# Kernel optimization log

Hardware: AMD Instinct MI355X
Metric: run time of the kernel (lower is better)

Reference implementation:

```python
import jax, jax.numpy as jnp
import numpy as np

N = 100000   # num nodes
E = 1000000  # num edges
IN = 64      # in_channels
H = 64       # hidden_dim
RESCUE_SCALE = 0.01


def setup_inputs() -> dict:
    key = jax.random.key(0)
    ks = jax.random.split(key, 8)
    x = jax.random.normal(ks[0], (N, IN), jnp.float32)
    edge_index = jax.random.randint(ks[1], (2, E), 0, N, dtype=jnp.int64)
    edge_weight = jax.random.uniform(ks[2], (E,), jnp.float32)
    glorot = lambda k, sh, fan: jax.random.normal(k, sh, jnp.float32) / np.sqrt(fan).astype(np.float32)
    W1 = glorot(ks[3], (IN, H), IN); b1 = jnp.zeros((H,), jnp.float32)
    W2 = glorot(ks[4], (H, H), H);  b2 = jnp.zeros((H,), jnp.float32)
    Wn = glorot(ks[5], (H, 1), H);  bn = jnp.zeros((1,), jnp.float32)
    Wr = glorot(ks[6], (H, 1), H);  br = jnp.zeros((1,), jnp.float32)
    return {"x": x, "edge_index": edge_index, "edge_weight": edge_weight,
            "W1": W1, "b1": b1, "W2": W2, "b2": b2,
            "Wn": Wn, "bn": bn, "Wr": Wr, "br": br}


def gcn_conv(x, src, dst, ew, W, b):
    # PyG GCNConv: linear first, then symmetric-normalized scatter-add aggregation.
    x = x @ W                                              # [N, H]
    deg = jax.ops.segment_sum(ew, dst, num_segments=N)     # weighted in-degree
    dinv = jnp.where(deg > 0, jax.lax.rsqrt(deg), 0.0)     # deg^{-1/2}, inf -> 0
    norm = dinv[src] * ew * dinv[dst]                      # [E+N]
    out = jax.ops.segment_sum(x[src] * norm[:, None], dst, num_segments=N)
    return out + b


def reference(x, edge_index, edge_weight, W1, b1, W2, b2, Wn, bn, Wr, br):
    # add self-loops with weight 1 (GCNConv default)
    loop = jnp.arange(N, dtype=edge_index.dtype)
    src = jnp.concatenate([edge_index[0], loop])
    dst = jnp.concatenate([edge_index[1], loop])
    ew = jnp.concatenate([edge_weight, jnp.ones((N,), edge_weight.dtype)])

    h = jax.nn.relu(gcn_conv(x, src, dst, ew, W1, b1))
    h = jax.nn.relu(gcn_conv(h, src, dst, ew, W2, b2))

    node_logits = (h @ Wn + bn).squeeze(-1)                # [N]
    node_selector = jax.nn.softmax(node_logits, axis=0)
    rescue_ratios = jax.nn.sigmoid((h @ Wr + br).squeeze(-1)) * RESCUE_SCALE
    return node_selector, rescue_ratios
```

## Files before the change

kernel.cpp:

```cpp
#include <hip/hip_runtime.h>
#include <hip/hip_fp16.h>
#include <math.h>

#define NN 100000
#define NE 1000000
#define CAP 32
#define OVCAP 4096
#define NEB 3907
#define NT32 3125
#define RB 256
#define GB1 512

typedef _Float16 half8 __attribute__((ext_vector_type(8)));
typedef float f32x4 __attribute__((ext_vector_type(4)));


__device__ __forceinline__ void stage_B_lds(const float* __restrict__ W,
                                            _Float16* __restrict__ ldsB) {
  for (int u = threadIdx.x; u < 512; u += 256) {
    int slane = u & 63, ts = u >> 6;
    int t = ts >> 1, s = ts & 1;
    int qq = slane >> 4, ll = slane & 15;
#pragma unroll
    for (int j = 0; j < 8; ++j)
      ldsB[u * 8 + j] = (_Float16)W[(s * 32 + qq * 8 + j) * 64 + t * 16 + ll];
  }
}


__global__ __launch_bounds__(256) void k_bucket_gemm1(const int* __restrict__ src,
                                                      const int* __restrict__ dst,
                                                      const float* __restrict__ ew,
                                                      const float* __restrict__ X,
                                                      const float* __restrict__ W1,
                                                      int* __restrict__ cnt,
                                                      int2* __restrict__ bucket,
                                                      int4* __restrict__ ovf,
                                                      int* __restrict__ ovf_n,
                                                      __half* __restrict__ Y) {
  __shared__ _Float16 ldsB[4096];
  if (blockIdx.x >= GB1) {
    int e = (blockIdx.x - GB1) * 256 + threadIdx.x;
    if (e < NE) {
      int s = src[e];
      int d = dst[e];
      float w = ew[e];
      int pos = atomicAdd(&cnt[d], 1);
      if (pos < CAP) {
        bucket[d * CAP + pos] = make_int2(s, __float_as_int(w));
      } else {
        int t = atomicAdd(ovf_n, 1);
        if (t < OVCAP) ovf[t] = make_int4(s, d, __float_as_int(w), 0);
      }
    }
    return;
  }
  stage_B_lds(W1, ldsB);
  __syncthreads();
  int lane = threadIdx.x & 63;
  int l15 = lane & 15, q = lane >> 4;
  half8 bfr[4][2];
#pragma unroll
  for (int t = 0; t < 4; ++t)
#pragma unroll
    for (int s = 0; s < 2; ++s)
      bfr[t][s] = *(half8*)&ldsB[((t * 2 + s) * 64 + lane) * 8];

  int wid = blockIdx.x * 4 + (threadIdx.x >> 6);
  for (int tile = wid; tile < NN / 16; tile += GB1 * 4) {
    int row = tile * 16 + l15;
    f32x4 acc[4] = {{0.f,0.f,0.f,0.f},{0.f,0.f,0.f,0.f},
                    {0.f,0.f,0.f,0.f},{0.f,0.f,0.f,0.f}};
#pragma unroll
    for (int s = 0; s < 2; ++s) {
      const float* ap = X + (size_t)row * 64 + s * 32 + q * 8;
      float4 a0 = *(const float4*)ap;
      float4 a1 = *(const float4*)(ap + 4);
      half8 af;
      af[0] = (_Float16)a0.x; af[1] = (_Float16)a0.y;
      af[2] = (_Float16)a0.z; af[3] = (_Float16)a0.w;
      af[4] = (_Float16)a1.x; af[5] = (_Float16)a1.y;
      af[6] = (_Float16)a1.z; af[7] = (_Float16)a1.w;
#pragma unroll
      for (int t = 0; t < 4; ++t)
        acc[t] = __builtin_amdgcn_mfma_f32_16x16x32_f16(af, bfr[t][s], acc[t], 0, 0, 0);
    }
#pragma unroll
    for (int r = 0; r < 4; ++r) {
      int rw = tile * 16 + q * 4 + r;
#pragma unroll
      for (int t = 0; t < 4; ++t)
        Y[(size_t)rw * 64 + t * 16 + l15] = __float2half(acc[t][r]);
    }
  }
}


__global__ __launch_bounds__(256) void k_dinv(const int* __restrict__ cnt,
                                              const int2* __restrict__ bucket,
                                              const int4* __restrict__ ovf,
                                              const int* __restrict__ ovf_n,
                                              float* __restrict__ dinv) {
  int t = threadIdx.x & 3;
  int node = blockIdx.x * 64 + (threadIdx.x >> 2);
  if (node >= NN) return;
  int c = cnt[node];
  int cc = c < CAP ? c : CAP;
  int nq = (cc + 1) >> 1;
  const int4* bk4 = (const int4*)(bucket + (size_t)node * CAP);
  float dsum = 0.f;
  for (int j = t; j < nq; j += 4) {
    int4 qv = bk4[j];
    int e0 = 2 * j, e1 = 2 * j + 1;
    if (e0 < cc) dsum += __int_as_float(qv.y);
    if (e1 < cc) dsum += __int_as_float(qv.w);
  }
  dsum += __shfl_xor(dsum, 1, 64);
  dsum += __shfl_xor(dsum, 2, 64);
  if (t == 0) {
    float tot = dsum + 1.0f;
    if (c > CAP) {
      int on = ovf_n[0]; if (on > OVCAP) on = OVCAP;
      for (int k = 0; k < on; ++k) {
        int4 o = ovf[k];
        if (o.y == node) tot += __int_as_float(o.z);
      }
    }
    dinv[node] = 1.0f / sqrtf(tot);
  }
}


__device__ __forceinline__ void h8load(const __half* p, float4& a, float4& b) {
  float4 raw = *(const float4*)p;
  __half2 h0 = *(__half2*)&raw.x;
  __half2 h1 = *(__half2*)&raw.y;
  __half2 h2 = *(__half2*)&raw.z;
  __half2 h3 = *(__half2*)&raw.w;
  float2 f0 = __half22float2(h0), f1 = __half22float2(h1);
  float2 f2 = __half22float2(h2), f3 = __half22float2(h3);
  a = make_float4(f0.x, f0.y, f1.x, f1.y);
  b = make_float4(f2.x, f2.y, f3.x, f3.y);
}

#define FMA8(xa, xb, v) do { \
  A.x = fmaf((xa).x, (v), A.x); A.y = fmaf((xa).y, (v), A.y); \
  A.z = fmaf((xa).z, (v), A.z); A.w = fmaf((xa).w, (v), A.w); \
  B.x = fmaf((xb).x, (v), B.x); B.y = fmaf((xb).y, (v), B.y); \
  B.z = fmaf((xb).z, (v), B.z); B.w = fmaf((xb).w, (v), B.w); } while (0)

template <bool FOLD>
__device__ __forceinline__ void gather_node8(const __half* __restrict__ xw,
                                             const int* __restrict__ cnt,
                                             const int2* __restrict__ bucket,
                                             const int4* __restrict__ ovf,
                                             const int* __restrict__ ovf_n,
                                             const float* __restrict__ dinv,
                                             int node, int l, float selfw,
                                             float4& A, float4& B) {
  int c = cnt[node];
  int cc = c < CAP ? c : CAP;
  const int4* bk4 = (const int4*)(bucket + (size_t)node * CAP);
  A = make_float4(0.f, 0.f, 0.f, 0.f);
  B = make_float4(0.f, 0.f, 0.f, 0.f);

  int j = 0;
  for (; j + 4 <= cc; j += 4) {
    int4 pa = bk4[j >> 1];
    int4 pb = bk4[(j >> 1) + 1];
    float4 xa0, xb0, xa1, xb1, xa2, xb2, xa3, xb3;
    h8load(xw + (size_t)pa.x * 64 + l * 8, xa0, xb0);
    h8load(xw + (size_t)pa.z * 64 + l * 8, xa1, xb1);
    h8load(xw + (size_t)pb.x * 64 + l * 8, xa2, xb2);
    h8load(xw + (size_t)pb.z * 64 + l * 8, xa3, xb3);
    float v0 = __int_as_float(pa.y);
    float v1 = __int_as_float(pa.w);
    float v2 = __int_as_float(pb.y);
    float v3 = __int_as_float(pb.w);
    if (FOLD) {
      v0 *= dinv[pa.x]; v1 *= dinv[pa.z];
      v2 *= dinv[pb.x]; v3 *= dinv[pb.z];
    }
    FMA8(xa0, xb0, v0);
    FMA8(xa1, xb1, v1);
    FMA8(xa2, xb2, v2);
    FMA8(xa3, xb3, v3);
  }
  const int2* bk = (const int2*)bk4;
  for (; j < cc; ++j) {
    int2 E = bk[j];
    float4 xa, xb;
    h8load(xw + (size_t)E.x * 64 + l * 8, xa, xb);
    float v = __int_as_float(E.y);
    if (FOLD) v *= dinv[E.x];
    FMA8(xa, xb, v);
  }
  if (c > CAP) {
    int on = ovf_n[0]; if (on > OVCAP) on = OVCAP;
    for (int t = 0; t < on; ++t) {
      int4 o = ovf[t];
      if (o.y == node) {
        float4 xa, xb;
        h8load(xw + (size_t)o.x * 64 + l * 8, xa, xb);
        float v = __int_as_float(o.z);
        if (FOLD) v *= dinv[o.x];
        FMA8(xa, xb, v);
      }
    }
  }
  {
    float4 xs, ys;
    h8load(xw + (size_t)node * 64 + l * 8, xs, ys);
    FMA8(xs, ys, selfw);
  }
}

#undef FMA8


__global__ __launch_bounds__(256) void k_gather_gemm2(const __half* __restrict__ xw,
                                                      const float* __restrict__ dinv,
                                                      const int* __restrict__ cnt,
                                                      const int2* __restrict__ bucket,
                                                      const int4* __restrict__ ovf,
                                                      const int* __restrict__ ovf_n,
                                                      const float* __restrict__ b1,
                                                      const float* __restrict__ W2,
                                                      __half* __restrict__ Y) {
  __shared__ _Float16 ldsB[4096];
  __shared__ _Float16 ldsR[32 * 72];
  __shared__ float sdi[32];
  stage_B_lds(W2, ldsB);

  int l = threadIdx.x & 7;
  int g = threadIdx.x >> 3;
  int node = blockIdx.x * 32 + g;
  float di = dinv[node];
  float4 A, Bv;
  gather_node8<true>(xw, cnt, bucket, ovf, ovf_n, dinv, node, l, di, A, Bv);
  const float4 ba = *(const float4*)(b1 + l * 8);
  const float4 bb = *(const float4*)(b1 + l * 8 + 4);
  _Float16* rp = &ldsR[g * 72 + l * 8];
  rp[0] = (_Float16)fmaxf(fmaf(A.x,  di, ba.x), 0.f);
  rp[1] = (_Float16)fmaxf(fmaf(A.y,  di, ba.y), 0.f);
  rp[2] = (_Float16)fmaxf(fmaf(A.z,  di, ba.z), 0.f);
  rp[3] = (_Float16)fmaxf(fmaf(A.w,  di, ba.w), 0.f);
  rp[4] = (_Float16)fmaxf(fmaf(Bv.x, di, bb.x), 0.f);
  rp[5] = (_Float16)fmaxf(fmaf(Bv.y, di, bb.y), 0.f);
  rp[6] = (_Float16)fmaxf(fmaf(Bv.z, di, bb.z), 0.f);
  rp[7] = (_Float16)fmaxf(fmaf(Bv.w, di, bb.w), 0.f);
  if (l == 0) sdi[g] = di;
  __syncthreads();

  int lane = threadIdx.x & 63;
  int l15 = lane & 15, q = lane >> 4;
  int t = threadIdx.x >> 6;
  half8 bf0 = *(half8*)&ldsB[((t * 2 + 0) * 64 + lane) * 8];
  half8 bf1 = *(half8*)&ldsB[((t * 2 + 1) * 64 + lane) * 8];
#pragma unroll
  for (int rt = 0; rt < 2; ++rt) {
    half8 a0 = *(half8*)&ldsR[(rt * 16 + l15) * 72 + q * 8];
    half8 a1 = *(half8*)&ldsR[(rt * 16 + l15) * 72 + 32 + q * 8];
    f32x4 acc2 = {0.f, 0.f, 0.f, 0.f};
    acc2 = __builtin_amdgcn_mfma_f32_16x16x32_f16(a0, bf0, acc2, 0, 0, 0);
    acc2 = __builtin_amdgcn_mfma_f32_16x16x32_f16(a1, bf1, acc2, 0, 0, 0);
#pragma unroll
    for (int r = 0; r < 4; ++r) {
      int rw = blockIdx.x * 32 + rt * 16 + q * 4 + r;
      float dv = sdi[rt * 16 + q * 4 + r];
      Y[(size_t)rw * 64 + t * 16 + l15] = __float2half(acc2[r] * dv);
    }
  }
}


__global__ __launch_bounds__(256) void k_gather_l2_heads(const __half* __restrict__ xw2,
                                                         const float* __restrict__ dinv,
                                                         const int* __restrict__ cnt,
                                                         const int2* __restrict__ bucket,
                                                         const int4* __restrict__ ovf,
                                                         const int* __restrict__ ovf_n,
                                                         const float* __restrict__ b2,
                                                         const float* __restrict__ Wn,
                                                         const float* __restrict__ bn,
                                                         const float* __restrict__ Wr,
                                                         const float* __restrict__ br,
                                                         float* __restrict__ logits,
                                                         float* __restrict__ rr,
                                                         float* __restrict__ part) {
  __shared__ float s[256];
  int l = threadIdx.x & 7;
  int node = blockIdx.x * 32 + (threadIdx.x >> 3);
  float4 A, Bv;
  gather_node8<false>(xw2, cnt, bucket, ovf, ovf_n, dinv, node, l, 1.0f, A, Bv);
  float di = dinv[node];
  const float4 ba = *(const float4*)(b2 + l * 8);
  const float4 bb = *(const float4*)(b2 + l * 8 + 4);
  float r0 = fmaxf(fmaf(A.x,  di, ba.x), 0.f);
  float r1 = fmaxf(fmaf(A.y,  di, ba.y), 0.f);
  float r2 = fmaxf(fmaf(A.z,  di, ba.z), 0.f);
  float r3 = fmaxf(fmaf(A.w,  di, ba.w), 0.f);
  float r4 = fmaxf(fmaf(Bv.x, di, bb.x), 0.f);
  float r5 = fmaxf(fmaf(Bv.y, di, bb.y), 0.f);
  float r6 = fmaxf(fmaf(Bv.z, di, bb.z), 0.f);
  float r7 = fmaxf(fmaf(Bv.w, di, bb.w), 0.f);
  const float4 wna = *(const float4*)(Wn + l * 8);
  const float4 wnb = *(const float4*)(Wn + l * 8 + 4);
  const float4 wra = *(const float4*)(Wr + l * 8);
  const float4 wrb = *(const float4*)(Wr + l * 8 + 4);
  float an = r0 * wna.x + r1 * wna.y + r2 * wna.z + r3 * wna.w
           + r4 * wnb.x + r5 * wnb.y + r6 * wnb.z + r7 * wnb.w;
  float ar = r0 * wra.x + r1 * wra.y + r2 * wra.z + r3 * wra.w
           + r4 * wrb.x + r5 * wrb.y + r6 * wrb.z + r7 * wrb.w;
#pragma unroll
  for (int m = 4; m > 0; m >>= 1) {
    an += __shfl_xor(an, m, 64);
    ar += __shfl_xor(ar, m, 64);
  }
  float lg = an + bn[0];
  if (l == 0) {
    logits[node] = lg;
    float xr = ar + br[0];
    rr[node] = 0.01f / (1.0f + expf(-xr));
  }
  s[threadIdx.x] = lg;
  __syncthreads();
  for (int w = 128; w > 0; w >>= 1) {
    if (threadIdx.x < w) s[threadIdx.x] = fmaxf(s[threadIdx.x], s[threadIdx.x + w]);
    __syncthreads();
  }
  if (threadIdx.x == 0) part[blockIdx.x] = s[0];
}


__global__ __launch_bounds__(256) void k_sexp(const float* __restrict__ logits,
                                              const float* __restrict__ part,
                                              float* __restrict__ sel,
                                              float* __restrict__ gsum) {
  __shared__ float s[256];
  float m = -INFINITY;
  for (int i = threadIdx.x; i < NT32; i += 256) m = fmaxf(m, part[i]);
  s[threadIdx.x] = m;
  __syncthreads();
  for (int w = 128; w > 0; w >>= 1) {
    if (threadIdx.x < w) s[threadIdx.x] = fmaxf(s[threadIdx.x], s[threadIdx.x + w]);
    __syncthreads();
  }
  float gm = s[0];
  __syncthreads();
  float acc = 0.0f;
  for (int i = blockIdx.x * 256 + threadIdx.x; i < NN; i += RB * 256) {
    float e = expf(logits[i] - gm);
    sel[i] = e;
    acc += e;
  }
  s[threadIdx.x] = acc;
  __syncthreads();
  for (int w = 128; w > 0; w >>= 1) {
    if (threadIdx.x < w) s[threadIdx.x] += s[threadIdx.x + w];
    __syncthreads();
  }
  if (threadIdx.x == 0) unsafeAtomicAdd(gsum, s[0]);
}

__global__ __launch_bounds__(256) void k_snorm(float* __restrict__ sel,
                                               const float* __restrict__ gsum) {
  int i = blockIdx.x * 256 + threadIdx.x;
  if (i < NN) sel[i] *= (1.0f / gsum[0]);
}


extern "C" void kernel_launch(void* const* d_in, const int* in_sizes, int n_in,
                              void* d_out, int out_size, void* d_ws, size_t ws_size,
                              hipStream_t stream) {
  const float* x  = (const float*)d_in[0];
  const int*   ei = (const int*)d_in[1];
  const float* ew = (const float*)d_in[2];
  const float* W1 = (const float*)d_in[3];
  const float* b1 = (const float*)d_in[4];
  const float* W2 = (const float*)d_in[5];
  const float* b2 = (const float*)d_in[6];
  const float* Wn = (const float*)d_in[7];
  const float* bn = (const float*)d_in[8];
  const float* Wr = (const float*)d_in[9];
  const float* br = (const float*)d_in[10];
  const int* src = ei;
  const int* dst = ei + NE;

  char* wsb = (char*)d_ws;
  __half* xw     = (__half*)wsb;
  __half* xw2    = (__half*)(wsb + 12800000);
  float*  logits = (float*)(wsb + 25600000);
  float*  dinv   = (float*)(wsb + 26000000);
  int2*   bucket = (int2*)(wsb + 26400000);
  int4*   ovf    = (int4*)(wsb + 52000000);
  int*    cnt    = (int*)(wsb + 52065536);
  int*    ovf_n  = (int*)(wsb + 52465536);
  float*  gsum   = (float*)(wsb + 52465540);
  float*  part1  = (float*)(wsb + 52465544);

  float* sel = (float*)d_out;
  float* rr  = (float*)d_out + NN;

  int gN = (NN + 255) / 256;

  hipMemsetAsync(cnt, 0, (size_t)(NN + 2) * 4, stream);

  k_bucket_gemm1<<<GB1 + NEB, 256, 0, stream>>>(src, dst, ew, x, W1,
                                                cnt, bucket, ovf, ovf_n, xw);

  k_dinv<<<(NN + 63) / 64, 256, 0, stream>>>(cnt, bucket, ovf, ovf_n, dinv);

  k_gather_gemm2<<<NT32, 256, 0, stream>>>(xw, dinv, cnt, bucket, ovf, ovf_n,
                                           b1, W2, xw2);

  k_gather_l2_heads<<<NT32, 256, 0, stream>>>(xw2, dinv, cnt, bucket, ovf, ovf_n,
                                              b2, Wn, bn, Wr, br, logits, rr, part1);

  k_sexp<<<RB, 256, 0, stream>>>(logits, part1, sel, gsum);
  k_snorm<<<gN, 256, 0, stream>>>(sel, gsum);
}
```

Baseline: 216.8 us.

## Gather two nodes per 8-lane group with predicated, interleaved neighbor loads

Each 8-lane group now aggregates two destination nodes at once, interleaving their bucket edge loads and masking out-of-range edges by redirecting them to a safe self index with zero weight. This raises memory-level parallelism in the gather, removes the scalar tail loop, and halves the block count (64 nodes per block), with each wave doing 4 MFMA column tiles instead of 2. The cost is wasted loads when the two nodes' degrees differ, higher register pressure, and bounds checks for the last partial block.

```diff
diff --git a/kernel.cpp b/kernel.cpp
--- a/kernel.cpp
+++ b/kernel.cpp
@@ -7,7 +7,7 @@
 #define CAP 32
 #define OVCAP 4096
 #define NEB 3907
-#define NT32 3125
+#define NB64 1563
 #define RB 256
 #define GB1 512
 
@@ -143,79 +143,76 @@
   b = make_float4(f2.x, f2.y, f3.x, f3.y);
 }
 
-#define FMA8(xa, xb, v) do { \
-  A.x = fmaf((xa).x, (v), A.x); A.y = fmaf((xa).y, (v), A.y); \
-  A.z = fmaf((xa).z, (v), A.z); A.w = fmaf((xa).w, (v), A.w); \
-  B.x = fmaf((xb).x, (v), B.x); B.y = fmaf((xb).y, (v), B.y); \
-  B.z = fmaf((xb).z, (v), B.z); B.w = fmaf((xb).w, (v), B.w); } while (0)
+__device__ __forceinline__ void fma8(float4& A, float4& B,
+                                     const float4& xa, const float4& xb, float v) {
+  A.x = fmaf(xa.x, v, A.x); A.y = fmaf(xa.y, v, A.y);
+  A.z = fmaf(xa.z, v, A.z); A.w = fmaf(xa.w, v, A.w);
+  B.x = fmaf(xb.x, v, B.x); B.y = fmaf(xb.y, v, B.y);
+  B.z = fmaf(xb.z, v, B.z); B.w = fmaf(xb.w, v, B.w);
+}
 
 template <bool FOLD>
-__device__ __forceinline__ void gather_node8(const __half* __restrict__ xw,
-                                             const int* __restrict__ cnt,
-                                             const int2* __restrict__ bucket,
-                                             const int4* __restrict__ ovf,
-                                             const int* __restrict__ ovf_n,
-                                             const float* __restrict__ dinv,
-                                             int node, int l, float selfw,
-                                             float4& A, float4& B) {
-  int c = cnt[node];
-  int cc = c < CAP ? c : CAP;
-  const int4* bk4 = (const int4*)(bucket + (size_t)node * CAP);
-  A = make_float4(0.f, 0.f, 0.f, 0.f);
-  B = make_float4(0.f, 0.f, 0.f, 0.f);
-
-  int j = 0;
-  for (; j + 4 <= cc; j += 4) {
-    int4 pa = bk4[j >> 1];
-    int4 pb = bk4[(j >> 1) + 1];
-    float4 xa0, xb0, xa1, xb1, xa2, xb2, xa3, xb3;
-    h8load(xw + (size_t)pa.x * 64 + l * 8, xa0, xb0);
-    h8load(xw + (size_t)pa.z * 64 + l * 8, xa1, xb1);
-    h8load(xw + (size_t)pb.x * 64 + l * 8, xa2, xb2);
-    h8load(xw + (size_t)pb.z * 64 + l * 8, xa3, xb3);
-    float v0 = __int_as_float(pa.y);
-    float v1 = __int_as_float(pa.w);
-    float v2 = __int_as_float(pb.y);
-    float v3 = __int_as_float(pb.w);
-    if (FOLD) {
-      v0 *= dinv[pa.x]; v1 *= dinv[pa.z];
-      v2 *= dinv[pb.x]; v3 *= dinv[pb.z];
-    }
-    FMA8(xa0, xb0, v0);
-    FMA8(xa1, xb1, v1);
-    FMA8(xa2, xb2, v2);
-    FMA8(xa3, xb3, v3);
-  }
-  const int2* bk = (const int2*)bk4;
-  for (; j < cc; ++j) {
-    int2 E = bk[j];
-    float4 xa, xb;
-    h8load(xw + (size_t)E.x * 64 + l * 8, xa, xb);
-    float v = __int_as_float(E.y);
-    if (FOLD) v *= dinv[E.x];
-    FMA8(xa, xb, v);
-  }
-  if (c > CAP) {
+__device__ __forceinline__ void edge_fma(const __half* __restrict__ xw,
+                                         const float* __restrict__ dinv,
+                                         int sidx, int wbits, bool ok, int safe,
+                                         int l, float4& A, float4& B) {
+  int s = ok ? sidx : safe;
+  float v = ok ? __int_as_float(wbits) : 0.0f;
+  if (FOLD) v *= dinv[s];
+  float4 xa, xb;
+  h8load(xw + (size_t)s * 64 + l * 8, xa, xb);
+  fma8(A, B, xa, xb, v);
+}
+
+template <bool FOLD>
+__device__ __forceinline__ void gather_dual(const __half* __restrict__ xw,
+                                            const int* __restrict__ cnt,
+                                            const int2* __restrict__ bucket,
+                                            const int4* __restrict__ ovf,
+                                            const int* __restrict__ ovf_n,
+                                            const float* __restrict__ dinv,
+                                            int nA, int nB, int l,
+                                            float swA, float swB,
+                                            float4& Aa, float4& Ab,
+                                            float4& Ba, float4& Bb) {
+  int cA = cnt[nA], cB = cnt[nB];
+  int ccA = cA < CAP ? cA : CAP;
+  int ccB = cB < CAP ? cB : CAP;
+  int ccM = ccA > ccB ? ccA : ccB;
+  const int4* bkA = (const int4*)(bucket + (size_t)nA * CAP);
+  const int4* bkB = (const int4*)(bucket + (size_t)nB * CAP);
+  Aa = make_float4(0.f, 0.f, 0.f, 0.f); Ab = Aa; Ba = Aa; Bb = Aa;
+
+  for (int j = 0; j < ccM; j += 4) {
+    int4 pa = bkA[j >> 1];
+    int4 qa = bkA[(j >> 1) + 1];
+    int4 pb = bkB[j >> 1];
+    int4 qb = bkB[(j >> 1) + 1];
+    edge_fma<FOLD>(xw, dinv, pa.x, pa.y, j + 0 < ccA, nA, l, Aa, Ab);
+    edge_fma<FOLD>(xw, dinv, pb.x, pb.y, j + 0 < ccB, nB, l, Ba, Bb);
+    edge_fma<FOLD>(xw, dinv, pa.z, pa.w, j + 1 < ccA, nA, l, Aa, Ab);
+    edge_fma<FOLD>(xw, dinv, pb.z, pb.w, j + 1 < ccB, nB, l, Ba, Bb);
+    edge_fma<FOLD>(xw, dinv, qa.x, qa.y, j + 2 < ccA, nA, l, Aa, Ab);
+    edge_fma<FOLD>(xw, dinv, qb.x, qb.y, j + 2 < ccB, nB, l, Ba, Bb);
+    edge_fma<FOLD>(xw, dinv, qa.z, qa.w, j + 3 < ccA, nA, l, Aa, Ab);
+    edge_fma<FOLD>(xw, dinv, qb.z, qb.w, j + 3 < ccB, nB, l, Ba, Bb);
+  }
+  if (cA > CAP || cB > CAP) {
     int on = ovf_n[0]; if (on > OVCAP) on = OVCAP;
     for (int t = 0; t < on; ++t) {
       int4 o = ovf[t];
-      if (o.y == node) {
-        float4 xa, xb;
-        h8load(xw + (size_t)o.x * 64 + l * 8, xa, xb);
-        float v = __int_as_float(o.z);
-        if (FOLD) v *= dinv[o.x];
-        FMA8(xa, xb, v);
-      }
+      if (o.y == nA) edge_fma<FOLD>(xw, dinv, o.x, o.z, true, nA, l, Aa, Ab);
+      if (o.y == nB) edge_fma<FOLD>(xw, dinv, o.x, o.z, true, nB, l, Ba, Bb);
     }
   }
   {
     float4 xs, ys;
-    h8load(xw + (size_t)node * 64 + l * 8, xs, ys);
-    FMA8(xs, ys, selfw);
-  }
-}
-
-#undef FMA8
+    h8load(xw + (size_t)nA * 64 + l * 8, xs, ys);
+    fma8(Aa, Ab, xs, ys, swA);
+    h8load(xw + (size_t)nB * 64 + l * 8, xs, ys);
+    fma8(Ba, Bb, xs, ys, swB);
+  }
+}
 
 
 __global__ __launch_bounds__(256) void k_gather_gemm2(const __half* __restrict__ xw,
@@ -228,47 +225,62 @@
                                                       const float* __restrict__ W2,
                                                       __half* __restrict__ Y) {
   __shared__ _Float16 ldsB[4096];
-  __shared__ _Float16 ldsR[32 * 72];
-  __shared__ float sdi[32];
+  __shared__ _Float16 ldsR[64 * 72];
+  __shared__ float sdi[64];
   stage_B_lds(W2, ldsB);
 
   int l = threadIdx.x & 7;
   int g = threadIdx.x >> 3;
-  int node = blockIdx.x * 32 + g;
-  float di = dinv[node];
-  float4 A, Bv;
-  gather_node8<true>(xw, cnt, bucket, ovf, ovf_n, dinv, node, l, di, A, Bv);
+  int nodeA = blockIdx.x * 64 + g * 2;
+  int nodeB = nodeA + 1;
+  int nA = nodeA < NN ? nodeA : NN - 1;
+  int nB = nodeB < NN ? nodeB : NN - 1;
+  float diA = dinv[nA], diB = dinv[nB];
+  float4 Aa, Ab, Ba, Bb;
+  gather_dual<true>(xw, cnt, bucket, ovf, ovf_n, dinv, nA, nB, l, diA, diB,
+                    Aa, Ab, Ba, Bb);
   const float4 ba = *(const float4*)(b1 + l * 8);
   const float4 bb = *(const float4*)(b1 + l * 8 + 4);
-  _Float16* rp = &ldsR[g * 72 + l * 8];
-  rp[0] = (_Float16)fmaxf(fmaf(A.x,  di, ba.x), 0.f);
-  rp[1] = (_Float16)fmaxf(fmaf(A.y,  di, ba.y), 0.f);
-  rp[2] = (_Float16)fmaxf(fmaf(A.z,  di, ba.z), 0.f);
-  rp[3] = (_Float16)fmaxf(fmaf(A.w,  di, ba.w), 0.f);
-  rp[4] = (_Float16)fmaxf(fmaf(Bv.x, di, bb.x), 0.f);
-  rp[5] = (_Float16)fmaxf(fmaf(Bv.y, di, bb.y), 0.f);
-  rp[6] = (_Float16)fmaxf(fmaf(Bv.z, di, bb.z), 0.f);
-  rp[7] = (_Float16)fmaxf(fmaf(Bv.w, di, bb.w), 0.f);
-  if (l == 0) sdi[g] = di;
+  _Float16* rpA = &ldsR[(g * 2) * 72 + l * 8];
+  rpA[0] = (_Float16)fmaxf(fmaf(Aa.x, diA, ba.x), 0.f);
+  rpA[1] = (_Float16)fmaxf(fmaf(Aa.y, diA, ba.y), 0.f);
+  rpA[2] = (_Float16)fmaxf(fmaf(Aa.z, diA, ba.z), 0.f);
+  rpA[3] = (_Float16)fmaxf(fmaf(Aa.w, diA, ba.w), 0.f);
+  rpA[4] = (_Float16)fmaxf(fmaf(Ab.x, diA, bb.x), 0.f);
+  rpA[5] = (_Float16)fmaxf(fmaf(Ab.y, diA, bb.y), 0.f);
+  rpA[6] = (_Float16)fmaxf(fmaf(Ab.z, diA, bb.z), 0.f);
+  rpA[7] = (_Float16)fmaxf(fmaf(Ab.w, diA, bb.w), 0.f);
+  _Float16* rpB = rpA + 72;
+  rpB[0] = (_Float16)fmaxf(fmaf(Ba.x, diB, ba.x), 0.f);
+  rpB[1] = (_Float16)fmaxf(fmaf(Ba.y, diB, ba.y), 0.f);
+  rpB[2] = (_Float16)fmaxf(fmaf(Ba.z, diB, ba.z), 0.f);
+  rpB[3] = (_Float16)fmaxf(fmaf(Ba.w, diB, ba.w), 0.f);
+  rpB[4] = (_Float16)fmaxf(fmaf(Bb.x, diB, bb.x), 0.f);
+  rpB[5] = (_Float16)fmaxf(fmaf(Bb.y, diB, bb.y), 0.f);
+  rpB[6] = (_Float16)fmaxf(fmaf(Bb.z, diB, bb.z), 0.f);
+  rpB[7] = (_Float16)fmaxf(fmaf(Bb.w, diB, bb.w), 0.f);
+  if (l == 0) { sdi[g * 2] = diA; sdi[g * 2 + 1] = diB; }
   __syncthreads();
 
   int lane = threadIdx.x & 63;
   int l15 = lane & 15, q = lane >> 4;
-  int t = threadIdx.x >> 6;
-  half8 bf0 = *(half8*)&ldsB[((t * 2 + 0) * 64 + lane) * 8];
-  half8 bf1 = *(half8*)&ldsB[((t * 2 + 1) * 64 + lane) * 8];
-#pragma unroll
-  for (int rt = 0; rt < 2; ++rt) {
-    half8 a0 = *(half8*)&ldsR[(rt * 16 + l15) * 72 + q * 8];
-    half8 a1 = *(half8*)&ldsR[(rt * 16 + l15) * 72 + 32 + q * 8];
+  int wv = threadIdx.x >> 6;
+  half8 a0 = *(half8*)&ldsR[(wv * 16 + l15) * 72 + q * 8];
+  half8 a1 = *(half8*)&ldsR[(wv * 16 + l15) * 72 + 32 + q * 8];
+#pragma unroll
+  for (int t = 0; t < 4; ++t) {
+    half8 bf0 = *(half8*)&ldsB[((t * 2 + 0) * 64 + lane) * 8];
+    half8 bf1 = *(half8*)&ldsB[((t * 2 + 1) * 64 + lane) * 8];
     f32x4 acc2 = {0.f, 0.f, 0.f, 0.f};
     acc2 = __builtin_amdgcn_mfma_f32_16x16x32_f16(a0, bf0, acc2, 0, 0, 0);
     acc2 = __builtin_amdgcn_mfma_f32_16x16x32_f16(a1, bf1, acc2, 0, 0, 0);
 #pragma unroll
     for (int r = 0; r < 4; ++r) {
-      int rw = blockIdx.x * 32 + rt * 16 + q * 4 + r;
-      float dv = sdi[rt * 16 + q * 4 + r];
-      Y[(size_t)rw * 64 + t * 16 + l15] = __float2half(acc2[r] * dv);
+      int rw = blockIdx.x * 64 + wv * 16 + q * 4 + r;
+      if (rw < NN) {
+        float dv = sdi[wv * 16 + q * 4 + r];
+        Y[(size_t)rw * 64 + t * 16 + l15] = __float2half(acc2[r] * dv);
+      }
     }
   }
 }
@@ -290,40 +302,68 @@
                                                          float* __restrict__ part) {
   __shared__ float s[256];
   int l = threadIdx.x & 7;
-  int node = blockIdx.x * 32 + (threadIdx.x >> 3);
-  float4 A, Bv;
-  gather_node8<false>(xw2, cnt, bucket, ovf, ovf_n, dinv, node, l, 1.0f, A, Bv);
-  float di = dinv[node];
+  int g = threadIdx.x >> 3;
+  int nodeA = blockIdx.x * 64 + g * 2;
+  int nodeB = nodeA + 1;
+  int nA = nodeA < NN ? nodeA : NN - 1;
+  int nB = nodeB < NN ? nodeB : NN - 1;
+  float4 Aa, Ab, Ba, Bb;
+  gather_dual<false>(xw2, cnt, bucket, ovf, ovf_n, dinv, nA, nB, l, 1.0f, 1.0f,
+                     Aa, Ab, Ba, Bb);
+  float diA = dinv[nA], diB = dinv[nB];
   const float4 ba = *(const float4*)(b2 + l * 8);
   const float4 bb = *(const float4*)(b2 + l * 8 + 4);
-  float r0 = fmaxf(fmaf(A.x,  di, ba.x), 0.f);
-  float r1 = fmaxf(fmaf(A.y,  di, ba.y), 0.f);
-  float r2 = fmaxf(fmaf(A.z,  di, ba.z), 0.f);
-  float r3 = fmaxf(fmaf(A.w,  di, ba.w), 0.f);
-  float r4 = fmaxf(fmaf(Bv.x, di, bb.x), 0.f);
-  float r5 = fmaxf(fmaf(Bv.y, di, bb.y), 0.f);
-  float r6 = fmaxf(fmaf(Bv.z, di, bb.z), 0.f);
-  float r7 = fmaxf(fmaf(Bv.w, di, bb.w), 0.f);
   const float4 wna = *(const float4*)(Wn + l * 8);
   const float4 wnb = *(const float4*)(Wn + l * 8 + 4);
   const float4 wra = *(const float4*)(Wr + l * 8);
   const float4 wrb = *(const float4*)(Wr + l * 8 + 4);
-  float an = r0 * wna.x + r1 * wna.y + r2 * wna.z + r3 * wna.w
-           + r4 * wnb.x + r5 * wnb.y + r6 * wnb.z + r7 * wnb.w;
-  float ar = r0 * wra.x + r1 * wra.y + r2 * wra.z + r3 * wra.w
-           + r4 * wrb.x + r5 * wrb.y + r6 * wrb.z + r7 * wrb.w;
+
+  float a0 = fmaxf(fmaf(Aa.x, diA, ba.x), 0.f);
+  float a1 = fmaxf(fmaf(Aa.y, diA, ba.y), 0.f);
+  float a2 = fmaxf(fmaf(Aa.z, diA, ba.z), 0.f);
+  float a3 = fmaxf(fmaf(Aa.w, diA, ba.w), 0.f);
+  float a4 = fmaxf(fmaf(Ab.x, diA, bb.x), 0.f);
+  float a5 = fmaxf(fmaf(Ab.y, diA, bb.y), 0.f);
+  float a6 = fmaxf(fmaf(Ab.z, diA, bb.z), 0.f);
+  float a7 = fmaxf(fmaf(Ab.w, diA, bb.w), 0.f);
+  float anA = a0 * wna.x + a1 * wna.y + a2 * wna.z + a3 * wna.w
+            + a4 * wnb.x + a5 * wnb.y + a6 * wnb.z + a7 * wnb.w;
+  float arA = a0 * wra.x + a1 * wra.y + a2 * wra.z + a3 * wra.w
+            + a4 * wrb.x + a5 * wrb.y + a6 * wrb.z + a7 * wrb.w;
+
+  float c0 = fmaxf(fmaf(Ba.x, diB, ba.x), 0.f);
+  float c1 = fmaxf(fmaf(Ba.y, diB, ba.y), 0.f);
+  float c2 = fmaxf(fmaf(Ba.z, diB, ba.z), 0.f);
+  float c3 = fmaxf(fmaf(Ba.w, diB, ba.w), 0.f);
+  float c4 = fmaxf(fmaf(Bb.x, diB, bb.x), 0.f);
+  float c5 = fmaxf(fmaf(Bb.y, diB, bb.y), 0.f);
+  float c6 = fmaxf(fmaf(Bb.z, diB, bb.z), 0.f);
+  float c7 = fmaxf(fmaf(Bb.w, diB, bb.w), 0.f);
+  float anB = c0 * wna.x + c1 * wna.y + c2 * wna.z + c3 * wna.w
+            + c4 * wnb.x + c5 * wnb.y + c6 * wnb.z + c7 * wnb.w;
+  float arB = c0 * wra.x + c1 * wra.y + c2 * wra.z + c3 * wra.w
+            + c4 * wrb.x + c5 * wrb.y + c6 * wrb.z + c7 * wrb.w;
+
 #pragma unroll
   for (int m = 4; m > 0; m >>= 1) {
-    an += __shfl_xor(an, m, 64);
-    ar += __shfl_xor(ar, m, 64);
-  }
-  float lg = an + bn[0];
+    anA += __shfl_xor(anA, m, 64);
+    arA += __shfl_xor(arA, m, 64);
+    anB += __shfl_xor(anB, m, 64);
+    arB += __shfl_xor(arB, m, 64);
+  }
+  float lgA = anA + bn[0];
+  float lgB = anB + bn[0];
   if (l == 0) {
-    logits[node] = lg;
-    float xr = ar + br[0];
-    rr[node] = 0.01f / (1.0f + expf(-xr));
-  }
-  s[threadIdx.x] = lg;
+    if (nodeA < NN) {
+      logits[nodeA] = lgA;
+      rr[nodeA] = 0.01f / (1.0f + expf(-(arA + br[0])));
+    }
+    if (nodeB < NN) {
+      logits[nodeB] = lgB;
+      rr[nodeB] = 0.01f / (1.0f + expf(-(arB + br[0])));
+    }
+  }
+  s[threadIdx.x] = fmaxf(lgA, lgB);
   __syncthreads();
   for (int w = 128; w > 0; w >>= 1) {
     if (threadIdx.x < w) s[threadIdx.x] = fmaxf(s[threadIdx.x], s[threadIdx.x + w]);
@@ -339,7 +379,7 @@
                                               float* __restrict__ gsum) {
   __shared__ float s[256];
   float m = -INFINITY;
-  for (int i = threadIdx.x; i < NT32; i += 256) m = fmaxf(m, part[i]);
+  for (int i = threadIdx.x; i < NB64; i += 256) m = fmaxf(m, part[i]);
   s[threadIdx.x] = m;
   __syncthreads();
   for (int w = 128; w > 0; w >>= 1) {
@@ -411,10 +451,10 @@
 
   k_dinv<<<(NN + 63) / 64, 256, 0, stream>>>(cnt, bucket, ovf, ovf_n, dinv);
 
-  k_gather_gemm2<<<NT32, 256, 0, stream>>>(xw, dinv, cnt, bucket, ovf, ovf_n,
+  k_gather_gemm2<<<NB64, 256, 0, stream>>>(xw, dinv, cnt, bucket, ovf, ovf_n,
                                            b1, W2, xw2);
 
-  k_gather_l2_heads<<<NT32, 256, 0, stream>>>(xw2, dinv, cnt, bucket, ovf, ovf_n,
+  k_gather_l2_heads<<<NB64, 256, 0, stream>>>(xw2, dinv, cnt, bucket, ovf, ovf_n,
                                               b2, Wn, bn, Wr, br, logits, rr, part1);
 
   k_sexp<<<RB, 256, 0, stream>>>(logits, part1, sel, gsum);
```

New measurement: 232.9 us. 1.07x slower.

## Partition edge bucketing by destination range per XCD with vectorized loads

Applied to the files above, without the earlier changes.

Bucketing blocks now each scan a chunk of 8192 edges using vectorized nontemporal loads, but only insert edges whose destination falls in one of eight node partitions chosen by block index. The aim is that blocks on the same XCD write atomics and buckets to a confined destination range, improving L2 locality of the scattered writes. In exchange, every edge is read eight times, which multiplies input read traffic.

```diff
diff --git a/kernel.cpp b/kernel.cpp
--- a/kernel.cpp
+++ b/kernel.cpp
@@ -6,13 +6,16 @@
 #define NE 1000000
 #define CAP 32
 #define OVCAP 4096
-#define NEB 3907
 #define NT32 3125
 #define RB 256
 #define GB1 512
+#define SB  1024
+#define PSZ 12500
 
 typedef _Float16 half8 __attribute__((ext_vector_type(8)));
 typedef float f32x4 __attribute__((ext_vector_type(4)));
+typedef int   iv4  __attribute__((ext_vector_type(4)));
+typedef float fv4  __attribute__((ext_vector_type(4)));
 
 
 __device__ __forceinline__ void stage_B_lds(const float* __restrict__ W,
@@ -40,17 +43,31 @@
                                                       __half* __restrict__ Y) {
   __shared__ _Float16 ldsB[4096];
   if (blockIdx.x >= GB1) {
-    int e = (blockIdx.x - GB1) * 256 + threadIdx.x;
-    if (e < NE) {
-      int s = src[e];
-      int d = dst[e];
-      float w = ew[e];
-      int pos = atomicAdd(&cnt[d], 1);
-      if (pos < CAP) {
-        bucket[d * CAP + pos] = make_int2(s, __float_as_int(w));
-      } else {
-        int t = atomicAdd(ovf_n, 1);
-        if (t < OVCAP) ovf[t] = make_int4(s, d, __float_as_int(w), 0);
+    int sb = blockIdx.x - GB1;
+    int p  = blockIdx.x & 7;
+    int kb = sb >> 3;
+    int lo = p * PSZ;
+    int base = kb * 8192 + (threadIdx.x << 2);
+#pragma unroll
+    for (int it = 0; it < 8; ++it) {
+      int e0 = base + it * 1024;
+      if (e0 < NE) {
+        iv4 d4 = __builtin_nontemporal_load((const iv4*)(dst + e0));
+        iv4 s4 = __builtin_nontemporal_load((const iv4*)(src + e0));
+        fv4 w4 = __builtin_nontemporal_load((const fv4*)(ew + e0));
+#pragma unroll
+        for (int u = 0; u < 4; ++u) {
+          int d = d4[u];
+          if ((unsigned)(d - lo) < (unsigned)PSZ) {
+            int pos = atomicAdd(&cnt[d], 1);
+            if (pos < CAP) {
+              bucket[d * CAP + pos] = make_int2(s4[u], __float_as_int(w4[u]));
+            } else {
+              int t = atomicAdd(ovf_n, 1);
+              if (t < OVCAP) ovf[t] = make_int4(s4[u], d, __float_as_int(w4[u]), 0);
+            }
+          }
+        }
       }
     }
     return;
@@ -406,8 +423,8 @@
 
   hipMemsetAsync(cnt, 0, (size_t)(NN + 2) * 4, stream);
 
-  k_bucket_gemm1<<<GB1 + NEB, 256, 0, stream>>>(src, dst, ew, x, W1,
-                                                cnt, bucket, ovf, ovf_n, xw);
+  k_bucket_gemm1<<<GB1 + SB, 256, 0, stream>>>(src, dst, ew, x, W1,
+                                               cnt, bucket, ovf, ovf_n, xw);
 
   k_dinv<<<(NN + 63) / 64, 256, 0, stream>>>(cnt, bucket, ovf, ovf_n, dinv);
 
```

Measured after the change: 222.2 us. 1.03x slower.
